# Optimization experiments

Measured on AMD Instinct MI355X. Metric: run time of the kernel, lower is better.

The kernel has to match this reference:

```python
import jax, jax.numpy as jnp
import numpy as np

EPS = 1e-7
BLOCK_SIZE = 128
LN_EPS = 1e-6

def _project(x):
    norm = jnp.maximum(jnp.linalg.norm(x, axis=-1, keepdims=True), EPS)
    max_norm = 1.0 - EPS
    return jnp.where(norm >= 1.0, x / norm * max_norm, x)

def _mobius_add(x, y, c):
    x2 = jnp.sum(x * x, -1, keepdims=True)
    y2 = jnp.sum(y * y, -1, keepdims=True)
    xy = jnp.sum(x * y, -1, keepdims=True)
    num = (1 + 2 * c * xy + c * y2) * x + (1 - c * x2) * y
    den = 1 + 2 * c * xy + c * c * x2 * y2
    return _project(num / jnp.maximum(den, EPS))

def _logmap0(y, c):
    sqrt_c = jnp.maximum(jnp.sqrt(c), EPS)
    y_norm = jnp.linalg.norm(y, axis=-1, keepdims=True)
    safe = jnp.maximum(y_norm, EPS)
    mag = jnp.arctanh(jnp.minimum(y_norm, 1.0 - EPS)) / sqrt_c
    return jnp.where(y_norm < EPS, jnp.zeros_like(y), mag * (y / safe))

def _expmap0(v, c):
    sqrt_c = jnp.maximum(jnp.sqrt(c), EPS)
    v_norm = jnp.linalg.norm(v, axis=-1, keepdims=True)
    safe = jnp.maximum(v_norm, EPS)
    mag = jnp.tanh(sqrt_c * safe) / sqrt_c
    return _project(jnp.where(v_norm < EPS, jnp.zeros_like(v), mag * (v / safe)))

def _dist(x, y, c):
    sqrt_c = jnp.maximum(jnp.sqrt(c), EPS)
    add_norm = jnp.linalg.norm(_mobius_add(-x, y, c), axis=-1)
    sc = jnp.squeeze(sqrt_c, -1)
    arg = jnp.minimum(sc * add_norm, 1.0 - EPS)
    return 2.0 * jnp.arctanh(arg) / sc

def _layernorm(t, scale, bias):
    mu = jnp.mean(t, -1, keepdims=True)
    var = jnp.mean((t - mu) ** 2, -1, keepdims=True)
    return (t - mu) * jax.lax.rsqrt(var + LN_EPS) * scale + bias

def _rope(x, fc):
    # x: [Be, H, bs, hd]; fc: [bs, hd//2] complex
    x_r, x_i = jnp.split(x, 2, -1)
    xc = jax.lax.complex(x_r, x_i)
    rot = xc * fc.reshape(1, 1, fc.shape[0], fc.shape[1])
    return jnp.concatenate([rot.real, rot.imag], -1)

def setup_inputs() -> dict:
    key = jax.random.key(0)
    ks = jax.random.split(key, 8)
    B, N, D, H = 1, 1024, 1024, 16
    w = lambda k, s: jax.random.normal(k, s, jnp.float32) * 0.02
    x = jax.random.normal(ks[0], (B, N, D), jnp.float32) * 0.02  # points inside the ball
    c_global = jax.random.uniform(ks[1], (B, 1), jnp.float32, minval=0.1, maxval=1.0)
    return dict(
        x=x, c_global=c_global,
        qkv_w=w(ks[2], (D, 3 * D)), qkv_b=jnp.zeros((3 * D,), jnp.float32),
        out_w=w(ks[3], (D, D)), out_b=jnp.zeros((D,), jnp.float32),
        ffn_w1=w(ks[4], (D, 4 * D)), ffn_b1=jnp.zeros((4 * D,), jnp.float32),
        ffn_w2=w(ks[5], (4 * D, D)), ffn_b2=jnp.zeros((D,), jnp.float32),
        ln1_scale=jnp.ones((D,), jnp.float32), ln1_bias=jnp.zeros((D,), jnp.float32),
        ln2_scale=jnp.ones((D,), jnp.float32), ln2_bias=jnp.zeros((D,), jnp.float32),
        c_logits=jnp.zeros((H,), jnp.float32),
        geo_scale=jnp.ones((1, H, 1, 1), jnp.float32),
        start_pos=0,
    )

def reference(x, c_global, qkv_w, qkv_b, out_w, out_b, ffn_w1, ffn_b1, ffn_w2, ffn_b2,
              ln1_scale, ln1_bias, ln2_scale, ln2_bias, c_logits, geo_scale, start_pos):
    B, N, D = x.shape
    H = c_logits.shape[0]
    hd = D // H
    bs = BLOCK_SIZE
    nb = N // bs
    Be = B * nb
    xb = x.reshape(Be, bs, D)
    c_b = jnp.repeat(c_global, nb, axis=0).reshape(Be, 1, 1)
    x_res1 = xb
    # tangent-space norm 1 + attention input
    x_norm = _expmap0(_layernorm(_logmap0(xb, c_b), ln1_scale, ln1_bias), c_b)
    x_tan = _logmap0(x_norm, c_b)
    qkv = (x_tan @ qkv_w + qkv_b).reshape(Be, bs, 3, H, hd).transpose(2, 0, 3, 1, 4)
    q, k, v = qkv[0], qkv[1], qkv[2]  # [Be, H, bs, hd]
    # block-local RoPE (module recomputes freqs_cis for h_dim/block_size internally)
    freqs = 1.0 / (10000.0 ** (jnp.arange(0, hd, 2, dtype=jnp.float32) / hd))
    fc = jnp.exp(1j * jnp.outer(jnp.arange(bs), freqs))
    q = _rope(q, fc)
    k = _rope(k, fc)
    c_head = jax.nn.softplus(c_logits).reshape(1, H, 1, 1)
    q_hyp = _expmap0(q, c_head)
    k_hyp = _expmap0(k, c_head)
    d = _dist(q_hyp[:, :, :, None, :], k_hyp[:, :, None, :, :], c_head[:, :, None, :, :])  # [Be,H,bs,bs]
    attn = jax.nn.softmax(-geo_scale * d, axis=-1)
    ao = jnp.einsum('bhqk,bhkd->bhqd', attn, v).transpose(0, 2, 1, 3).reshape(Be, bs, D)
    ao = ao @ out_w + out_b
    x_att = _mobius_add(x_res1, _expmap0(ao, c_b), c_b)
    # tangent-space norm 2 + hyperbolic FFN
    x_norm2 = _expmap0(_layernorm(_logmap0(x_att, c_b), ln2_scale, ln2_bias), c_b)
    t = _logmap0(x_norm2, c_b)
    t = jax.nn.gelu(t @ ffn_w1 + ffn_b1) @ ffn_w2 + ffn_b2
    x_ffn = _expmap0(t, c_b)
    out = _mobius_add(x_att, x_ffn, c_b)
    return out.reshape(B, N, D)
```

## Files before the change

kernel.cpp:

```cpp
#include <hip/hip_runtime.h>

typedef unsigned int uint;
typedef unsigned short ushort;
typedef __attribute__((ext_vector_type(8))) short bf16x8;
typedef __attribute__((ext_vector_type(4))) float f32x4;

#define EPSF 1e-7f
#define ONE_M_EPS 0.99999988079071044921875f
#define ATANH_1ME 8.4056213f
#define Y2_CLIP 0.99999982f

__device__ __forceinline__ ushort f2bf(float f){
  union{float f;uint u;}x; x.f=f; uint u=x.u;
  return (ushort)((u + 0x7fffu + ((u>>16)&1u)) >> 16);
}
__device__ __forceinline__ float bf2f(ushort u){
  union{uint u;float f;}x; x.u = ((uint)u)<<16; return x.f;
}
__device__ __forceinline__ float atanh_c(float a){
  a = fminf(a, ONE_M_EPS);
  return 0.5f*__logf((1.f+a)/(1.f-a));
}
__device__ __forceinline__ float gelu_t(float v){
  return 0.5f*v*(1.f + tanhf(0.7978845608f*(v + 0.044715f*v*v*v)));
}

__device__ __forceinline__ float expmap_factor(float n2, float sc, float& r2){
  float n = sqrtf(n2);
  if (n < EPSF) { r2 = 0.f; return 0.f; }
  float mag = tanhf(sc*n)/sc;
  float f = mag/n;
  if (mag >= 1.f) { f *= ONE_M_EPS/mag; r2 = Y2_CLIP; }
  else r2 = mag*mag;
  return f;
}
__device__ __forceinline__ float roundtrip_factor(float tn2, float sc){
  float tn = sqrtf(tn2);
  if (tn < EPSF) return 0.f;
  float mag = tanhf(sc*tn)/sc;
  if (mag >= 1.f) {
    return ATANH_1ME / (sc * tn);
  } else {
    if (mag < EPSF) return 0.f;
    return (mag/tn) * (atanh_c(mag) / (sc * mag));
  }
}

__device__ __constant__ float FREQS[32] = {
  1.0f, 0.7498942093324559f, 0.5623413251903491f, 0.4216965034285822f,
  0.31622776601683794f, 0.23713737056616552f, 0.1778279410038923f, 0.13335214321633242f,
  0.1f, 0.07498942093324558f, 0.05623413251903491f, 0.04216965034285822f,
  0.03162277660168379f, 0.023713737056616554f, 0.01778279410038923f, 0.013335214321633242f,
  0.01f, 0.007498942093324559f, 0.005623413251903491f, 0.004216965034285822f,
  0.0031622776601683794f, 0.0023713737056616554f, 0.0017782794100389228f, 0.0013335214321633241f,
  0.001f, 0.0007498942093324558f, 0.0005623413251903491f, 0.0004216965034285822f,
  0.00031622776601683794f, 0.00023713737056616553f, 0.00017782794100389227f, 0.00013335214321633243f
};

__device__ __forceinline__ void rope64(float* v, int row){
  #pragma unroll
  for (int i=0;i<32;i++){
    float sn, cn; __sincosf((float)row * FREQS[i], &sn, &cn);
    float a = v[i], b = v[i+32];
    v[i] = a*cn - b*sn;
    v[i+32] = a*sn + b*cn;
  }
}

__device__ __forceinline__ float blkSum(float v, float* tmp){
  #pragma unroll
  for (int o=32;o>0;o>>=1) v += __shfl_xor(v, o, 64);
  int w = threadIdx.x >> 6;
  if ((threadIdx.x & 63) == 0) tmp[w] = v;
  __syncthreads();
  v = tmp[0]+tmp[1]+tmp[2]+tmp[3];
  __syncthreads();
  return v;
}
__device__ __forceinline__ float2 blkSum2(float a, float b, float* tmp){
  #pragma unroll
  for (int o=32;o>0;o>>=1){ a += __shfl_xor(a, o, 64); b += __shfl_xor(b, o, 64); }
  int w = threadIdx.x >> 6;
  if ((threadIdx.x & 63) == 0){ tmp[w] = a; tmp[4+w] = b; }
  __syncthreads();
  float2 r; r.x = tmp[0]+tmp[1]+tmp[2]+tmp[3]; r.y = tmp[4]+tmp[5]+tmp[6]+tmp[7];
  __syncthreads();
  return r;
}

__global__ __launch_bounds__(256) void k_pre(const float* __restrict__ qkv_w,
    const float* __restrict__ out_w, const float* __restrict__ ffn_w1,
    const float* __restrict__ ffn_w2, const float* __restrict__ x,
    const float* __restrict__ cg, const float* __restrict__ lns, const float* __restrict__ lnb,
    ushort* __restrict__ wq, ushort* __restrict__ wo,
    ushort* __restrict__ w1, ushort* __restrict__ w2, ushort* __restrict__ xtan){
  __shared__ float s[32][33];
  int b = blockIdx.x;
  if (b < 12288){
    const float* W; ushort* WT; int K, N;
    if (b < 3072){ W=qkv_w; WT=wq; K=1024; N=3072; }
    else if (b < 4096){ b-=3072; W=out_w; WT=wo; K=1024; N=1024; }
    else if (b < 8192){ b-=4096; W=ffn_w1; WT=w1; K=1024; N=4096; }
    else { b-=8192; W=ffn_w2; WT=w2; K=4096; N=1024; }
    int nbn = N >> 5;
    int n0 = (b % nbn)*32, k0 = (b / nbn)*32;
    int tx = threadIdx.x & 31, ty = threadIdx.x >> 5;
    #pragma unroll
    for (int i=0;i<4;i++)
      s[ty+8*i][tx] = W[(size_t)(k0+ty+8*i)*N + n0+tx];
    __syncthreads();
    #pragma unroll
    for (int i=0;i<4;i++)
      WT[(size_t)(n0+ty+8*i)*K + k0+tx] = f2bf(s[tx][ty+8*i]);
  } else {
    float* tmp = &s[0][0];
    int r = b - 12288, t = threadIdx.x;
    float c = cg[0];
    float sc = fmaxf(sqrtf(c), EPSF);
    float4 xv = ((const float4*)(x + (size_t)r*1024))[t];
    float n2 = blkSum(xv.x*xv.x + xv.y*xv.y + xv.z*xv.z + xv.w*xv.w, tmp);
    float n = sqrtf(n2);
    float f1 = (n < EPSF) ? 0.f : (atanh_c(n) / sc / n);
    float ux = xv.x*f1, uy = xv.y*f1, uz = xv.z*f1, uw = xv.w*f1;
    float2 s12 = blkSum2(ux+uy+uz+uw, ux*ux+uy*uy+uz*uz+uw*uw, tmp);
    float mu = s12.x*(1.f/1024.f);
    float var = s12.y*(1.f/1024.f) - mu*mu;
    float inv = rsqrtf(var + 1e-6f);
    float4 sv = ((const float4*)lns)[t];
    float4 bv = ((const float4*)lnb)[t];
    float ta = (ux-mu)*inv*sv.x + bv.x;
    float tb = (uy-mu)*inv*sv.y + bv.y;
    float tc = (uz-mu)*inv*sv.z + bv.z;
    float td = (uw-mu)*inv*sv.w + bv.w;
    float tn2 = blkSum(ta*ta+tb*tb+tc*tc+td*td, tmp);
    float f = roundtrip_factor(tn2, sc);
    ushort4 o; o.x=f2bf(ta*f); o.y=f2bf(tb*f); o.z=f2bf(tc*f); o.w=f2bf(td*f);
    ((ushort4*)(xtan + (size_t)r*1024))[t] = o;
  }
}

template<int EPI>
__global__ __launch_bounds__(256) void k_gemm(const ushort* __restrict__ A,
    const ushort* __restrict__ Bt, const float* __restrict__ bias,
    void* __restrict__ C, int M, int N, int Kstride, int Kchunk){
  constexpr int MF = 2, NF = 4;
  __shared__ ushort As[2][128*64];
  __shared__ ushort Bs[2][64*64];
  const int tid = threadIdx.x;
  const int lane = tid & 63;
  const int wid = tid >> 6;
  const int ro = wid * 32, co = 0;
  const int l15 = lane & 15, hi = lane >> 4;
  const int nwg = gridDim.x * gridDim.y;
  const int lin = blockIdx.y * gridDim.x + blockIdx.x;
  const int qq = nwg >> 3, rr = nwg & 7;
  const int xcd = lin & 7, ii = lin >> 3;
  const int swz = (xcd < rr) ? (xcd*(qq+1) + ii) : (rr*(qq+1) + (xcd-rr)*qq + ii);
  const int m0 = (swz % gridDim.y) * 128;
  const int n0 = (swz / gridDim.y) * 64;
  const int z = blockIdx.z;
  const int kbase = z * Kchunk;
  const int swr = (l15 & 7) << 3;

  f32x4 acc[MF][NF];
  #pragma unroll
  for (int i=0;i<MF;i++)
    #pragma unroll
    for (int j=0;j<NF;j++) acc[i][j] = (f32x4){0.f,0.f,0.f,0.f};

  auto stage = [&](int buf, int koff){
    #pragma unroll
    for (int r2=0;r2<4;r2++){
      int idx = r2*256 + tid;
      int row = idx >> 3, cc = idx & 7;
      int off = koff + ((cc ^ (row & 7)) << 3);
      const ushort* ga = A + (size_t)(m0+row)*Kstride + off;
      int lo = (r2*256 + (tid & 192)) * 8;
      __builtin_amdgcn_global_load_lds((const __attribute__((address_space(1))) uint*)ga,
          (__attribute__((address_space(3))) uint*)&As[buf][lo], 16, 0, 0);
    }
    #pragma unroll
    for (int r2=0;r2<2;r2++){
      int idx = r2*256 + tid;
      int row = idx >> 3, cc = idx & 7;
      int off = koff + ((cc ^ (row & 7)) << 3);
      const ushort* gb = Bt + (size_t)(n0+row)*Kstride + off;
      int lo = (r2*256 + (tid & 192)) * 8;
      __builtin_amdgcn_global_load_lds((const __attribute__((address_space(1))) uint*)gb,
          (__attribute__((address_space(3))) uint*)&Bs[buf][lo], 16, 0, 0);
    }
  };
  auto compute = [&](int buf){
    #pragma unroll
    for (int ks=0;ks<2;ks++){
      bf16x8 af[MF], bfv[NF];
      int cb = (ks*32 + hi*8) ^ swr;
      #pragma unroll
      for (int m2=0;m2<MF;m2++) af[m2]  = *(const bf16x8*)&As[buf][(ro+m2*16+l15)*64 + cb];
      #pragma unroll
      for (int n2=0;n2<NF;n2++) bfv[n2] = *(const bf16x8*)&Bs[buf][(co+n2*16+l15)*64 + cb];
      #pragma unroll
      for (int m2=0;m2<MF;m2++)
        #pragma unroll
        for (int n2=0;n2<NF;n2++)
          acc[m2][n2] = __builtin_amdgcn_mfma_f32_16x16x32_bf16(af[m2], bfv[n2], acc[m2][n2], 0, 0, 0);
    }
  };

  const int nt = Kchunk >> 6;
  stage(0, kbase);
  __syncthreads();
  int cur = 0;
  for (int t = 1; t < nt; ++t){
    stage(cur ^ 1, kbase + t*64);
    compute(cur);
    __syncthreads();
    cur ^= 1;
  }
  compute(cur);

  #pragma unroll
  for (int m=0;m<MF;m++){
    #pragma unroll
    for (int n=0;n<NF;n++){
      int gc = n0 + co + n*16 + l15;
      float bb = (EPI == 3) ? (z == 0 ? bias[gc] : 0.f) : bias[gc];
      #pragma unroll
      for (int i=0;i<4;i++){
        int gr = m0 + ro + m*16 + hi*4 + i;
        float v = acc[m][n][i] + bb;
        if (EPI == 2) v = gelu_t(v);
        if (EPI == 2) ((ushort*)C)[(size_t)gr*N + gc] = f2bf(v);
        else ((float*)C)[(size_t)z*M*N + (size_t)gr*N + gc] = v;
      }
    }
  }
}

__global__ __launch_bounds__(256) void k_attn5(const float* __restrict__ qkv,
    const float* __restrict__ c_logits, const float* __restrict__ geo,
    ushort* __restrict__ ao){
  constexpr size_t PSTRIDE = (size_t)1024*3072;
  __shared__ ushort Kh[128*64], Kl[128*64];
  __shared__ ushort Vth[64*128];
  __shared__ ushort Qh[64*64], Ql[64*64];
  __shared__ float k2s[128], q2s[64];
  const int h = blockIdx.x, be = blockIdx.y, qs = blockIdx.z;
  const int tid = threadIdx.x;
  const float cl = c_logits[h];
  const float ch = (cl > 20.f) ? cl : log1pf(__expf(cl));
  const float sc = fmaxf(sqrtf(ch), EPSF);
  const float gs = geo[h];

  if (tid < 128){
    int kv = tid;
    const float4* pa = (const float4*)(qkv + (size_t)(be*128+kv)*3072 + 1024 + h*64);
    const float4* pb = (const float4*)(qkv + PSTRIDE + (size_t)(be*128+kv)*3072 + 1024 + h*64);
    float v[64];
    #pragma unroll
    for (int c=0;c<16;c++){
      float4 ta = pa[c], tb = pb[c];
      v[4*c]=ta.x+tb.x; v[4*c+1]=ta.y+tb.y; v[4*c+2]=ta.z+tb.z; v[4*c+3]=ta.w+tb.w;
    }
    rope64(v, kv);
    float n2 = 0.f;
    #pragma unroll
    for (int e=0;e<64;e++) n2 += v[e]*v[e];
    float r2; float f = expmap_factor(n2, sc, r2);
    k2s[kv] = r2;
    #pragma unroll
    for (int cch=0; cch<8; cch++){
      uint hw[4], lw[4];
      #pragma unroll
      for (int w2=0; w2<4; w2++){
        float a0 = v[cch*8 + w2*2] * f, a1 = v[cch*8 + w2*2 + 1] * f;
        ushort h0 = f2bf(a0); ushort l0 = f2bf(a0 - bf2f(h0));
        ushort h1 = f2bf(a1); ushort l1 = f2bf(a1 - bf2f(h1));
        hw[w2] = (uint)h0 | ((uint)h1<<16);
        lw[w2] = (uint)l0 | ((uint)l1<<16);
      }
      uint4 uh; uh.x=hw[0]; uh.y=hw[1]; uh.z=hw[2]; uh.w=hw[3];
      uint4 ul; ul.x=lw[0]; ul.y=lw[1]; ul.z=lw[2]; ul.w=lw[3];
      int idx = kv*64 + ((cch ^ (kv&7))<<3);
      *(uint4*)&Kh[idx] = uh;
      *(uint4*)&Kl[idx] = ul;
    }
  } else if (tid < 192){
    #pragma unroll
    for (int rr2=0; rr2<2; rr2++){
      int kv = (tid - 128) + rr2*64;
      const float4* pa = (const float4*)(qkv + (size_t)(be*128+kv)*3072 + 2048 + h*64);
      const float4* pb = (const float4*)(qkv + PSTRIDE + (size_t)(be*128+kv)*3072 + 2048 + h*64);
      float v[64];
      #pragma unroll
      for (int c=0;c<16;c++){
        float4 ta = pa[c], tb = pb[c];
        v[4*c]=ta.x+tb.x; v[4*c+1]=ta.y+tb.y; v[4*c+2]=ta.z+tb.z; v[4*c+3]=ta.w+tb.w;
      }
      #pragma unroll
      for (int d=0; d<64; d++){
        int idx = d*128 + (((kv>>3) ^ (d&7))<<3) + (kv&7);
        Vth[idx] = f2bf(v[d]);
      }
    }
  } else {
    int ql = tid - 192;
    int qrow = qs*64 + ql;
    const float4* pa = (const float4*)(qkv + (size_t)(be*128+qrow)*3072 + h*64);
    const float4* pb = (const float4*)(qkv + PSTRIDE + (size_t)(be*128+qrow)*3072 + h*64);
    float v[64];
    #pragma unroll
    for (int c=0;c<16;c++){
      float4 ta = pa[c], tb = pb[c];
      v[4*c]=ta.x+tb.x; v[4*c+1]=ta.y+tb.y; v[4*c+2]=ta.z+tb.z; v[4*c+3]=ta.w+tb.w;
    }
    rope64(v, qrow);
    float n2 = 0.f;
    #pragma unroll
    for (int e=0;e<64;e++) n2 += v[e]*v[e];
    float r2; float f = expmap_factor(n2, sc, r2);
    q2s[ql] = r2;
    #pragma unroll
    for (int cch=0; cch<8; cch++){
      uint hw[4], lw[4];
      #pragma unroll
      for (int w2=0; w2<4; w2++){
        float a0 = v[cch*8 + w2*2] * f, a1 = v[cch*8 + w2*2 + 1] * f;
        ushort h0 = f2bf(a0); ushort l0 = f2bf(a0 - bf2f(h0));
        ushort h1 = f2bf(a1); ushort l1 = f2bf(a1 - bf2f(h1));
        hw[w2] = (uint)h0 | ((uint)h1<<16);
        lw[w2] = (uint)l0 | ((uint)l1<<16);
      }
      uint4 uh; uh.x=hw[0]; uh.y=hw[1]; uh.z=hw[2]; uh.w=hw[3];
      uint4 ul; ul.x=lw[0]; ul.y=lw[1]; ul.z=lw[2]; ul.w=lw[3];
      int idx = ql*64 + ((cch ^ (ql&7))<<3);
      *(uint4*)&Qh[idx] = uh;
      *(uint4*)&Ql[idx] = ul;
    }
  }
  __syncthreads();

  const int lane = tid & 63, w = tid >> 6;
  const int l15 = lane & 15, hi4 = lane >> 4;
  f32x4 acc[8];
  #pragma unroll
  for (int nf=0;nf<8;nf++) acc[nf] = (f32x4){0.f,0.f,0.f,0.f};
  #pragma unroll
  for (int ks=0; ks<2; ks++){
    int qrowL = w*16 + l15;
    int qidx = qrowL*64 + (((ks*4 + hi4) ^ (qrowL&7))<<3);
    bf16x8 qh = *(const bf16x8*)&Qh[qidx];
    bf16x8 ql2 = *(const bf16x8*)&Ql[qidx];
    #pragma unroll
    for (int nf=0; nf<8; nf++){
      int krow = nf*16 + l15;
      int kidx = krow*64 + (((ks*4 + hi4) ^ (krow&7))<<3);
      bf16x8 kh = *(const bf16x8*)&Kh[kidx];
      bf16x8 kl2 = *(const bf16x8*)&Kl[kidx];
      acc[nf] = __builtin_amdgcn_mfma_f32_16x16x32_bf16(qh, kh, acc[nf], 0, 0, 0);
      acc[nf] = __builtin_amdgcn_mfma_f32_16x16x32_bf16(qh, kl2, acc[nf], 0, 0, 0);
      acc[nf] = __builtin_amdgcn_mfma_f32_16x16x32_bf16(ql2, kh, acc[nf], 0, 0, 0);
    }
  }
  __syncthreads();

  float q2v[4], Bfv[4];
  #pragma unroll
  for (int i=0;i<4;i++){ q2v[i] = q2s[w*16 + hi4*4 + i]; Bfv[i] = 1.f - ch*q2v[i]; }
  const float e2 = 2.f*ch;
  #pragma unroll
  for (int nf=0; nf<8; nf++){
    float k2 = k2s[nf*16 + l15];
    #pragma unroll
    for (int i=0;i<4;i++){
      float xy = acc[nf][i];
      float Af = 1.f + ch*k2 - e2*xy;
      float den = fmaxf(Af - ch*k2*Bfv[i], EPSF);
      float num2 = fmaxf(Af*(Af*q2v[i] - 2.f*Bfv[i]*xy) + Bfv[i]*Bfv[i]*k2, 0.f);
      float rn = sqrtf(num2)/den;
      rn = (rn >= 1.f) ? ONE_M_EPS : rn;
      float arg = fminf(sc*rn, ONE_M_EPS);
      float dd = __logf((1.f+arg)/(1.f-arg)) / sc;
      acc[nf][i] = -gs*dd;
    }
  }
  #pragma unroll
  for (int i=0;i<4;i++){
    float m = acc[0][i];
    #pragma unroll
    for (int nf=1;nf<8;nf++) m = fmaxf(m, acc[nf][i]);
    #pragma unroll
    for (int o=1;o<16;o<<=1) m = fmaxf(m, __shfl_xor(m, o));
    float l = 0.f;
    #pragma unroll
    for (int nf=0;nf<8;nf++){ float pp = __expf(acc[nf][i]-m); acc[nf][i] = pp; l += pp; }
    #pragma unroll
    for (int o=1;o<16;o<<=1) l += __shfl_xor(l, o);
    float inv = 1.f/l;
    #pragma unroll
    for (int nf=0;nf<8;nf++){
      float p = acc[nf][i]*inv;
      ushort ph = f2bf(p);
      ushort pl = f2bf(p - bf2f(ph));
      int row = w*16 + hi4*4 + i, col = nf*16 + l15;
      int idx = row*128 + (((col>>3) ^ (row&7))<<3) + (col&7);
      Kh[idx] = ph; Kl[idx] = pl;
    }
  }
  __syncthreads();

  f32x4 acc2[4];
  #pragma unroll
  for (int nf=0;nf<4;nf++) acc2[nf] = (f32x4){0.f,0.f,0.f,0.f};
  #pragma unroll
  for (int ks=0; ks<4; ks++){
    int prow = w*16 + l15;
    int pidx = prow*128 + (((ks*4 + hi4) ^ (prow&7))<<3);
    bf16x8 ph = *(const bf16x8*)&Kh[pidx];
    bf16x8 pl = *(const bf16x8*)&Kl[pidx];
    #pragma unroll
    for (int nf=0; nf<4; nf++){
      int vrow = nf*16 + l15;
      int vidx = vrow*128 + (((ks*4 + hi4) ^ (vrow&7))<<3);
      bf16x8 vh = *(const bf16x8*)&Vth[vidx];
      acc2[nf] = __builtin_amdgcn_mfma_f32_16x16x32_bf16(ph, vh, acc2[nf], 0, 0, 0);
      acc2[nf] = __builtin_amdgcn_mfma_f32_16x16x32_bf16(pl, vh, acc2[nf], 0, 0, 0);
    }
  }
  #pragma unroll
  for (int nf=0; nf<4; nf++)
    #pragma unroll
    for (int i=0;i<4;i++){
      int row = qs*64 + w*16 + hi4*4 + i;
      int col = nf*16 + l15;
      ao[(size_t)(be*128 + row)*1024 + h*64 + col] = f2bf(acc2[nf][i]);
    }
}

__global__ __launch_bounds__(256) void k_postattn(const float* __restrict__ x,
    const float* __restrict__ proj, const float* __restrict__ cg,
    const float* __restrict__ lns, const float* __restrict__ lnb,
    float* __restrict__ xatt, ushort* __restrict__ tout){
  __shared__ float tmp[8];
  int r = blockIdx.x, t = threadIdx.x;
  float c = cg[0], sc = fmaxf(sqrtf(c), EPSF);
  float4 pa = ((const float4*)(proj + (size_t)r*1024))[t];
  float4 pb = ((const float4*)(proj + 1024*1024 + (size_t)r*1024))[t];
  float4 pc = ((const float4*)(proj + 2*1024*1024 + (size_t)r*1024))[t];
  float4 pd = ((const float4*)(proj + 3*1024*1024 + (size_t)r*1024))[t];
  float4 pv; pv.x=(pa.x+pb.x)+(pc.x+pd.x); pv.y=(pa.y+pb.y)+(pc.y+pd.y);
  pv.z=(pa.z+pb.z)+(pc.z+pd.z); pv.w=(pa.w+pb.w)+(pc.w+pd.w);
  float4 xv = ((const float4*)(x + (size_t)r*1024))[t];
  float pn2 = blkSum(pv.x*pv.x+pv.y*pv.y+pv.z*pv.z+pv.w*pv.w, tmp);
  float y2; float fy = expmap_factor(pn2, sc, y2);
  float ya = pv.x*fy, yb = pv.y*fy, yc = pv.z*fy, yd = pv.w*fy;
  float2 s = blkSum2(xv.x*xv.x+xv.y*xv.y+xv.z*xv.z+xv.w*xv.w,
                     xv.x*ya+xv.y*yb+xv.z*yc+xv.w*yd, tmp);
  float x2 = s.x, xy = s.y;
  float Af = 1.f + 2.f*c*xy + c*y2;
  float Bf = 1.f - c*x2;
  float den = fmaxf(1.f + 2.f*c*xy + c*c*x2*y2, EPSF);
  float num2 = fmaxf(Af*Af*x2 + 2.f*Af*Bf*xy + Bf*Bf*y2, 0.f);
  float rn = sqrtf(num2)/den;
  float fp = (rn >= 1.f) ? (ONE_M_EPS/fmaxf(rn,EPSF)) : 1.f;
  float xan = (rn >= 1.f) ? ONE_M_EPS : rn;
  float g = fp/den;
  float xa = (Af*xv.x + Bf*ya)*g;
  float xb = (Af*xv.y + Bf*yb)*g;
  float xc = (Af*xv.z + Bf*yc)*g;
  float xd = (Af*xv.w + Bf*yd)*g;
  float4 xo; xo.x=xa; xo.y=xb; xo.z=xc; xo.w=xd;
  ((float4*)(xatt + (size_t)r*1024))[t] = xo;
  float at = (rn >= 1.f) ? ATANH_1ME : atanh_c(xan);
  float fl = (xan < EPSF) ? 0.f : at / sc / fmaxf(xan, EPSF);
  float ux = xa*fl, uy = xb*fl, uz = xc*fl, uw = xd*fl;
  float2 s12 = blkSum2(ux+uy+uz+uw, ux*ux+uy*uy+uz*uz+uw*uw, tmp);
  float mu = s12.x*(1.f/1024.f);
  float var = s12.y*(1.f/1024.f) - mu*mu;
  float inv = rsqrtf(var + 1e-6f);
  float4 sv = ((const float4*)lns)[t];
  float4 bv = ((const float4*)lnb)[t];
  float ta = (ux-mu)*inv*sv.x + bv.x;
  float tb = (uy-mu)*inv*sv.y + bv.y;
  float tc = (uz-mu)*inv*sv.z + bv.z;
  float td = (uw-mu)*inv*sv.w + bv.w;
  float tn2 = blkSum(ta*ta+tb*tb+tc*tc+td*td, tmp);
  float f = roundtrip_factor(tn2, sc);
  ushort4 o; o.x=f2bf(ta*f); o.y=f2bf(tb*f); o.z=f2bf(tc*f); o.w=f2bf(td*f);
  ((ushort4*)(tout + (size_t)r*1024))[t] = o;
}

__global__ __launch_bounds__(256) void k_final(const float* __restrict__ xatt,
    const float* __restrict__ tf, const float* __restrict__ cg, float* __restrict__ out){
  __shared__ float tmp[8];
  int r = blockIdx.x, t = threadIdx.x;
  float c = cg[0], sc = fmaxf(sqrtf(c), EPSF);
  float4 fa = ((const float4*)(tf + (size_t)r*1024))[t];
  float4 fb = ((const float4*)(tf + 1024*1024 + (size_t)r*1024))[t];
  float4 fc = ((const float4*)(tf + 2*1024*1024 + (size_t)r*1024))[t];
  float4 fd = ((const float4*)(tf + 3*1024*1024 + (size_t)r*1024))[t];
  float4 fv; fv.x=(fa.x+fb.x)+(fc.x+fd.x); fv.y=(fa.y+fb.y)+(fc.y+fd.y);
  fv.z=(fa.z+fb.z)+(fc.z+fd.z); fv.w=(fa.w+fb.w)+(fc.w+fd.w);
  float4 xv = ((const float4*)(xatt + (size_t)r*1024))[t];
  float fn2 = blkSum(fv.x*fv.x+fv.y*fv.y+fv.z*fv.z+fv.w*fv.w, tmp);
  float y2; float fy = expmap_factor(fn2, sc, y2);
  float ya = fv.x*fy, yb = fv.y*fy, yc = fv.z*fy, yd = fv.w*fy;
  float2 s = blkSum2(xv.x*xv.x+xv.y*xv.y+xv.z*xv.z+xv.w*xv.w,
                     xv.x*ya+xv.y*yb+xv.z*yc+xv.w*yd, tmp);
  float x2 = s.x, xy = s.y;
  float Af = 1.f + 2.f*c*xy + c*y2;
  float Bf = 1.f - c*x2;
  float den = fmaxf(1.f + 2.f*c*xy + c*c*x2*y2, EPSF);
  float num2 = fmaxf(Af*Af*x2 + 2.f*Af*Bf*xy + Bf*Bf*y2, 0.f);
  float rn = sqrtf(num2)/den;
  float fp = (rn >= 1.f) ? (ONE_M_EPS/fmaxf(rn,EPSF)) : 1.f;
  float g = fp/den;
  float4 o;
  o.x = (Af*xv.x + Bf*ya)*g;
  o.y = (Af*xv.y + Bf*yb)*g;
  o.z = (Af*xv.z + Bf*yc)*g;
  o.w = (Af*xv.w + Bf*yd)*g;
  ((float4*)(out + (size_t)r*1024))[t] = o;
}

extern "C" void kernel_launch(void* const* d_in, const int* in_sizes, int n_in,
                              void* d_out, int out_size, void* d_ws, size_t ws_size,
                              hipStream_t stream){
  (void)in_sizes; (void)n_in; (void)out_size; (void)ws_size;
  const float* x     = (const float*)d_in[0];
  const float* cg    = (const float*)d_in[1];
  const float* qkv_w = (const float*)d_in[2];
  const float* qkv_b = (const float*)d_in[3];
  const float* out_w = (const float*)d_in[4];
  const float* out_b = (const float*)d_in[5];
  const float* ffn_w1= (const float*)d_in[6];
  const float* ffn_b1= (const float*)d_in[7];
  const float* ffn_w2= (const float*)d_in[8];
  const float* ffn_b2= (const float*)d_in[9];
  const float* ln1s  = (const float*)d_in[10];
  const float* ln1b  = (const float*)d_in[11];
  const float* ln2s  = (const float*)d_in[12];
  const float* ln2b  = (const float*)d_in[13];
  const float* clog  = (const float*)d_in[14];
  const float* geo   = (const float*)d_in[15];

  char* p = (char*)d_ws;
  auto take = [&](size_t n){ char* r = p; p += (n + 255) & ~(size_t)255; return r; };
  ushort* wt_qkv  = (ushort*)take((size_t)3072*1024*2);
  ushort* wt_out  = (ushort*)take((size_t)1024*1024*2);
  ushort* wt_ffn1 = (ushort*)take((size_t)4096*1024*2);
  ushort* wt_ffn2 = (ushort*)take((size_t)1024*4096*2);
  float*  bufA    = (float*)take((size_t)2*1024*3072*4);
  ushort* bufB    = (ushort*)take((size_t)1024*1024*2);
  float*  bufC    = (float*)take((size_t)4*1024*1024*4);
  float*  xatt    = (float*)take((size_t)1024*1024*4);
  ushort* tbuf    = (ushort*)take((size_t)1024*1024*2);

  k_pre<<<13312, 256, 0, stream>>>(qkv_w, out_w, ffn_w1, ffn_w2, x, cg, ln1s, ln1b,
                                   wt_qkv, wt_out, wt_ffn1, wt_ffn2, bufB);
  k_gemm<3><<<dim3(48,8,2), 256, 0, stream>>>(bufB, wt_qkv, qkv_b, (void*)bufA, 1024, 3072, 1024, 512);
  k_attn5<<<dim3(16,8,2), 256, 0, stream>>>(bufA, clog, geo, bufB);
  k_gemm<3><<<dim3(16,8,4), 256, 0, stream>>>(bufB, wt_out, out_b, (void*)bufC, 1024, 1024, 1024, 256);
  k_postattn<<<1024, 256, 0, stream>>>(x, bufC, cg, ln2s, ln2b, xatt, tbuf);
  k_gemm<2><<<dim3(64,8,1), 256, 0, stream>>>(tbuf, wt_ffn1, ffn_b1, (void*)bufA, 1024, 4096, 1024, 1024);
  k_gemm<3><<<dim3(16,8,4), 256, 0, stream>>>((const ushort*)bufA, wt_ffn2, ffn_b2, (void*)bufC, 1024, 1024, 4096, 1024);
  k_final<<<1024, 256, 0, stream>>>(xatt, bufC, cg, (float*)d_out);
}
```

Before: 116.6 us.

## Fuse RoPE, expmap and hi/lo split into QKV GEMM epilogue

The QKV GEMM drops its split-K of 2 and gains an epilogue that adds bias, applies RoPE, computes per-row norms with the expmap scale, and writes Q/K as bf16 hi/lo pairs plus V as bf16 in per-head layouts. The attention kernel then loads these tiles straight into LDS with global_load_lds instead of reading and summing two fp32 partial buffers and redoing the preprocessing. This removes the fp32 QKV round trip and the duplicated per-block Q/K work. In exchange the GEMM epilogue gets heavier, its stores are scattered 2-byte writes, and the GEMM loses the parallelism of split-K.

```diff
diff --git a/kernel.cpp b/kernel.cpp
--- a/kernel.cpp
+++ b/kernel.cpp
@@ -56,16 +56,6 @@
   0.001f, 0.0007498942093324558f, 0.0005623413251903491f, 0.0004216965034285822f,
   0.00031622776601683794f, 0.00023713737056616553f, 0.00017782794100389227f, 0.00013335214321633243f
 };
-
-__device__ __forceinline__ void rope64(float* v, int row){
-  #pragma unroll
-  for (int i=0;i<32;i++){
-    float sn, cn; __sincosf((float)row * FREQS[i], &sn, &cn);
-    float a = v[i], b = v[i+32];
-    v[i] = a*cn - b*sn;
-    v[i+32] = a*sn + b*cn;
-  }
-}
 
 __device__ __forceinline__ float blkSum(float v, float* tmp){
   #pragma unroll
@@ -142,14 +132,18 @@
 template<int EPI>
 __global__ __launch_bounds__(256) void k_gemm(const ushort* __restrict__ A,
     const ushort* __restrict__ Bt, const float* __restrict__ bias,
-    void* __restrict__ C, int M, int N, int Kstride, int Kchunk){
+    void* __restrict__ C, int M, int N, int Kstride, int Kchunk,
+    ushort* __restrict__ qhg, ushort* __restrict__ qlg,
+    ushort* __restrict__ khg, ushort* __restrict__ klg,
+    ushort* __restrict__ vhg, float* __restrict__ q2g, float* __restrict__ k2g,
+    const float* __restrict__ clog){
   constexpr int MF = 2, NF = 4;
   __shared__ ushort As[2][128*64];
   __shared__ ushort Bs[2][64*64];
   const int tid = threadIdx.x;
   const int lane = tid & 63;
   const int wid = tid >> 6;
-  const int ro = wid * 32, co = 0;
+  const int ro = wid * 32;
   const int l15 = lane & 15, hi = lane >> 4;
   const int nwg = gridDim.x * gridDim.y;
   const int lin = blockIdx.y * gridDim.x + blockIdx.x;
@@ -198,7 +192,7 @@
       #pragma unroll
       for (int m2=0;m2<MF;m2++) af[m2]  = *(const bf16x8*)&As[buf][(ro+m2*16+l15)*64 + cb];
       #pragma unroll
-      for (int n2=0;n2<NF;n2++) bfv[n2] = *(const bf16x8*)&Bs[buf][(co+n2*16+l15)*64 + cb];
+      for (int n2=0;n2<NF;n2++) bfv[n2] = *(const bf16x8*)&Bs[buf][(n2*16+l15)*64 + cb];
       #pragma unroll
       for (int m2=0;m2<MF;m2++)
         #pragma unroll
@@ -219,28 +213,103 @@
   }
   compute(cur);
 
+  if (EPI == 4){
+    float v[MF][NF][4];
+    #pragma unroll
+    for (int m2=0;m2<MF;m2++)
+      #pragma unroll
+      for (int n2=0;n2<NF;n2++){
+        float bb = bias[n0 + n2*16 + l15];
+        #pragma unroll
+        for (int i=0;i<4;i++) v[m2][n2][i] = acc[m2][n2][i] + bb;
+      }
+    const int type = n0 >> 10;
+    const int h = (n0 & 1023) >> 6;
+    if (type < 2){
+      #pragma unroll
+      for (int m2=0;m2<MF;m2++)
+        #pragma unroll
+        for (int i=0;i<4;i++){
+          int gr = m0 + ro + m2*16 + hi*4 + i;
+          float r = (float)(gr & 127);
+          #pragma unroll
+          for (int pp=0;pp<2;pp++){
+            int d = pp*16 + l15;
+            float sn, cn; __sincosf(r * FREQS[d], &sn, &cn);
+            float a = v[m2][pp][i], b = v[m2][pp+2][i];
+            v[m2][pp][i]   = a*cn - b*sn;
+            v[m2][pp+2][i] = a*sn + b*cn;
+          }
+        }
+      const float cl = clog[h];
+      const float chh = (cl > 20.f) ? cl : log1pf(__expf(cl));
+      const float sch = fmaxf(sqrtf(chh), EPSF);
+      ushort* hdst = (type==0) ? qhg : khg;
+      ushort* ldst = (type==0) ? qlg : klg;
+      float*  sdst = (type==0) ? q2g : k2g;
+      #pragma unroll
+      for (int m2=0;m2<MF;m2++)
+        #pragma unroll
+        for (int i=0;i<4;i++){
+          float n2s = 0.f;
+          #pragma unroll
+          for (int n2=0;n2<NF;n2++) n2s += v[m2][n2][i]*v[m2][n2][i];
+          #pragma unroll
+          for (int o=1;o<16;o<<=1) n2s += __shfl_xor(n2s, o);
+          float r2; float f = expmap_factor(n2s, sch, r2);
+          int gr = m0 + ro + m2*16 + hi*4 + i;
+          int be = gr >> 7, r = gr & 127;
+          size_t rowbase = ((size_t)(be*16 + h)*128 + r)*64;
+          #pragma unroll
+          for (int n2=0;n2<NF;n2++){
+            float val = v[m2][n2][i]*f;
+            ushort hb = f2bf(val);
+            ushort lb = f2bf(val - bf2f(hb));
+            hdst[rowbase + n2*16 + l15] = hb;
+            ldst[rowbase + n2*16 + l15] = lb;
+          }
+          if (l15 == 0) sdst[(size_t)(be*16+h)*128 + r] = r2;
+        }
+    } else {
+      #pragma unroll
+      for (int m2=0;m2<MF;m2++)
+        #pragma unroll
+        for (int i=0;i<4;i++){
+          int gr = m0 + ro + m2*16 + hi*4 + i;
+          int be = gr >> 7, r = gr & 127;
+          size_t rowbase = ((size_t)(be*16 + h)*128 + r)*64;
+          #pragma unroll
+          for (int n2=0;n2<NF;n2++)
+            vhg[rowbase + n2*16 + l15] = f2bf(v[m2][n2][i]);
+        }
+    }
+    return;
+  }
+
   #pragma unroll
   for (int m=0;m<MF;m++){
     #pragma unroll
     for (int n=0;n<NF;n++){
-      int gc = n0 + co + n*16 + l15;
+      int gc = n0 + n*16 + l15;
       float bb = (EPI == 3) ? (z == 0 ? bias[gc] : 0.f) : bias[gc];
       #pragma unroll
       for (int i=0;i<4;i++){
         int gr = m0 + ro + m*16 + hi*4 + i;
-        float v = acc[m][n][i] + bb;
-        if (EPI == 2) v = gelu_t(v);
-        if (EPI == 2) ((ushort*)C)[(size_t)gr*N + gc] = f2bf(v);
-        else ((float*)C)[(size_t)z*M*N + (size_t)gr*N + gc] = v;
+        float v2 = acc[m][n][i] + bb;
+        if (EPI == 2) v2 = gelu_t(v2);
+        if (EPI == 2) ((ushort*)C)[(size_t)gr*N + gc] = f2bf(v2);
+        else ((float*)C)[(size_t)z*M*N + (size_t)gr*N + gc] = v2;
       }
     }
   }
 }
 
-__global__ __launch_bounds__(256) void k_attn5(const float* __restrict__ qkv,
+__global__ __launch_bounds__(256) void k_attn6(const ushort* __restrict__ qhg,
+    const ushort* __restrict__ qlg, const ushort* __restrict__ khg,
+    const ushort* __restrict__ klg, const ushort* __restrict__ vhg,
+    const float* __restrict__ q2g, const float* __restrict__ k2g,
     const float* __restrict__ c_logits, const float* __restrict__ geo,
     ushort* __restrict__ ao){
-  constexpr size_t PSTRIDE = (size_t)1024*3072;
   __shared__ ushort Kh[128*64], Kl[128*64];
   __shared__ ushort Vth[64*128];
   __shared__ ushort Qh[64*64], Ql[64*64];
@@ -251,92 +320,45 @@
   const float ch = (cl > 20.f) ? cl : log1pf(__expf(cl));
   const float sc = fmaxf(sqrtf(ch), EPSF);
   const float gs = geo[h];
-
+  const size_t tbase = (size_t)(be*16 + h)*8192;
+
+  #pragma unroll
+  for (int r2=0;r2<4;r2++){
+    int idx = r2*256 + tid;
+    int row = idx >> 3, cc = idx & 7;
+    int off = row*64 + ((cc ^ (row & 7)) << 3);
+    int lo = (r2*256 + (tid & 192)) * 8;
+    __builtin_amdgcn_global_load_lds((const __attribute__((address_space(1))) uint*)(khg + tbase + off),
+        (__attribute__((address_space(3))) uint*)&Kh[lo], 16, 0, 0);
+    __builtin_amdgcn_global_load_lds((const __attribute__((address_space(1))) uint*)(klg + tbase + off),
+        (__attribute__((address_space(3))) uint*)&Kl[lo], 16, 0, 0);
+  }
+  #pragma unroll
+  for (int r2=0;r2<2;r2++){
+    int idx = r2*256 + tid;
+    int row = idx >> 3, cc = idx & 7;
+    int off = (qs*64 + row)*64 + ((cc ^ (row & 7)) << 3);
+    int lo = (r2*256 + (tid & 192)) * 8;
+    __builtin_amdgcn_global_load_lds((const __attribute__((address_space(1))) uint*)(qhg + tbase + off),
+        (__attribute__((address_space(3))) uint*)&Qh[lo], 16, 0, 0);
+    __builtin_amdgcn_global_load_lds((const __attribute__((address_space(1))) uint*)(qlg + tbase + off),
+        (__attribute__((address_space(3))) uint*)&Ql[lo], 16, 0, 0);
+  }
   if (tid < 128){
     int kv = tid;
-    const float4* pa = (const float4*)(qkv + (size_t)(be*128+kv)*3072 + 1024 + h*64);
-    const float4* pb = (const float4*)(qkv + PSTRIDE + (size_t)(be*128+kv)*3072 + 1024 + h*64);
-    float v[64];
-    #pragma unroll
-    for (int c=0;c<16;c++){
-      float4 ta = pa[c], tb = pb[c];
-      v[4*c]=ta.x+tb.x; v[4*c+1]=ta.y+tb.y; v[4*c+2]=ta.z+tb.z; v[4*c+3]=ta.w+tb.w;
-    }
-    rope64(v, kv);
-    float n2 = 0.f;
-    #pragma unroll
-    for (int e=0;e<64;e++) n2 += v[e]*v[e];
-    float r2; float f = expmap_factor(n2, sc, r2);
-    k2s[kv] = r2;
-    #pragma unroll
-    for (int cch=0; cch<8; cch++){
-      uint hw[4], lw[4];
-      #pragma unroll
-      for (int w2=0; w2<4; w2++){
-        float a0 = v[cch*8 + w2*2] * f, a1 = v[cch*8 + w2*2 + 1] * f;
-        ushort h0 = f2bf(a0); ushort l0 = f2bf(a0 - bf2f(h0));
-        ushort h1 = f2bf(a1); ushort l1 = f2bf(a1 - bf2f(h1));
-        hw[w2] = (uint)h0 | ((uint)h1<<16);
-        lw[w2] = (uint)l0 | ((uint)l1<<16);
-      }
-      uint4 uh; uh.x=hw[0]; uh.y=hw[1]; uh.z=hw[2]; uh.w=hw[3];
-      uint4 ul; ul.x=lw[0]; ul.y=lw[1]; ul.z=lw[2]; ul.w=lw[3];
-      int idx = kv*64 + ((cch ^ (kv&7))<<3);
-      *(uint4*)&Kh[idx] = uh;
-      *(uint4*)&Kl[idx] = ul;
-    }
+    const uint4* src = (const uint4*)(vhg + tbase + kv*64);
+    ushort v[64];
+    #pragma unroll
+    for (int c2=0;c2<8;c2++) *(uint4*)&v[c2*8] = src[c2];
+    #pragma unroll
+    for (int d=0; d<64; d++){
+      int idx = d*128 + (((kv>>3) ^ (d&7))<<3) + (kv&7);
+      Vth[idx] = v[d];
+    }
+    k2s[kv] = k2g[(size_t)(be*16+h)*128 + kv];
   } else if (tid < 192){
-    #pragma unroll
-    for (int rr2=0; rr2<2; rr2++){
-      int kv = (tid - 128) + rr2*64;
-      const float4* pa = (const float4*)(qkv + (size_t)(be*128+kv)*3072 + 2048 + h*64);
-      const float4* pb = (const float4*)(qkv + PSTRIDE + (size_t)(be*128+kv)*3072 + 2048 + h*64);
-      float v[64];
-      #pragma unroll
-      for (int c=0;c<16;c++){
-        float4 ta = pa[c], tb = pb[c];
-        v[4*c]=ta.x+tb.x; v[4*c+1]=ta.y+tb.y; v[4*c+2]=ta.z+tb.z; v[4*c+3]=ta.w+tb.w;
-      }
-      #pragma unroll
-      for (int d=0; d<64; d++){
-        int idx = d*128 + (((kv>>3) ^ (d&7))<<3) + (kv&7);
-        Vth[idx] = f2bf(v[d]);
-      }
-    }
-  } else {
-    int ql = tid - 192;
-    int qrow = qs*64 + ql;
-    const float4* pa = (const float4*)(qkv + (size_t)(be*128+qrow)*3072 + h*64);
-    const float4* pb = (const float4*)(qkv + PSTRIDE + (size_t)(be*128+qrow)*3072 + h*64);
-    float v[64];
-    #pragma unroll
-    for (int c=0;c<16;c++){
-      float4 ta = pa[c], tb = pb[c];
-      v[4*c]=ta.x+tb.x; v[4*c+1]=ta.y+tb.y; v[4*c+2]=ta.z+tb.z; v[4*c+3]=ta.w+tb.w;
-    }
-    rope64(v, qrow);
-    float n2 = 0.f;
-    #pragma unroll
-    for (int e=0;e<64;e++) n2 += v[e]*v[e];
-    float r2; float f = expmap_factor(n2, sc, r2);
-    q2s[ql] = r2;
-    #pragma unroll
-    for (int cch=0; cch<8; cch++){
-      uint hw[4], lw[4];
-      #pragma unroll
-      for (int w2=0; w2<4; w2++){
-        float a0 = v[cch*8 + w2*2] * f, a1 = v[cch*8 + w2*2 + 1] * f;
-        ushort h0 = f2bf(a0); ushort l0 = f2bf(a0 - bf2f(h0));
-        ushort h1 = f2bf(a1); ushort l1 = f2bf(a1 - bf2f(h1));
-        hw[w2] = (uint)h0 | ((uint)h1<<16);
-        lw[w2] = (uint)l0 | ((uint)l1<<16);
-      }
-      uint4 uh; uh.x=hw[0]; uh.y=hw[1]; uh.z=hw[2]; uh.w=hw[3];
-      uint4 ul; ul.x=lw[0]; ul.y=lw[1]; ul.z=lw[2]; ul.w=lw[3];
-      int idx = ql*64 + ((cch ^ (ql&7))<<3);
-      *(uint4*)&Qh[idx] = uh;
-      *(uint4*)&Ql[idx] = ul;
-    }
+    int i2 = tid - 128;
+    q2s[i2] = q2g[(size_t)(be*16+h)*128 + qs*64 + i2];
   }
   __syncthreads();
 
@@ -550,19 +572,30 @@
   ushort* wt_out  = (ushort*)take((size_t)1024*1024*2);
   ushort* wt_ffn1 = (ushort*)take((size_t)4096*1024*2);
   ushort* wt_ffn2 = (ushort*)take((size_t)1024*4096*2);
-  float*  bufA    = (float*)take((size_t)2*1024*3072*4);
+  float*  bufA    = (float*)take((size_t)1024*4096*4);
   ushort* bufB    = (ushort*)take((size_t)1024*1024*2);
   float*  bufC    = (float*)take((size_t)4*1024*1024*4);
   float*  xatt    = (float*)take((size_t)1024*1024*4);
   ushort* tbuf    = (ushort*)take((size_t)1024*1024*2);
+  ushort* qhg     = (ushort*)take((size_t)1024*1024*2);
+  ushort* qlg     = (ushort*)take((size_t)1024*1024*2);
+  ushort* khg     = (ushort*)take((size_t)1024*1024*2);
+  ushort* klg     = (ushort*)take((size_t)1024*1024*2);
+  ushort* vhg     = (ushort*)take((size_t)1024*1024*2);
+  float*  q2g     = (float*)take((size_t)16384*4);
+  float*  k2g     = (float*)take((size_t)16384*4);
 
   k_pre<<<13312, 256, 0, stream>>>(qkv_w, out_w, ffn_w1, ffn_w2, x, cg, ln1s, ln1b,
                                    wt_qkv, wt_out, wt_ffn1, wt_ffn2, bufB);
-  k_gemm<3><<<dim3(48,8,2), 256, 0, stream>>>(bufB, wt_qkv, qkv_b, (void*)bufA, 1024, 3072, 1024, 512);
-  k_attn5<<<dim3(16,8,2), 256, 0, stream>>>(bufA, clog, geo, bufB);
-  k_gemm<3><<<dim3(16,8,4), 256, 0, stream>>>(bufB, wt_out, out_b, (void*)bufC, 1024, 1024, 1024, 256);
+  k_gemm<4><<<dim3(48,8,1), 256, 0, stream>>>(bufB, wt_qkv, qkv_b, nullptr, 1024, 3072, 1024, 1024,
+                                              qhg, qlg, khg, klg, vhg, q2g, k2g, clog);
+  k_attn6<<<dim3(16,8,2), 256, 0, stream>>>(qhg, qlg, khg, klg, vhg, q2g, k2g, clog, geo, bufB);
+  k_gemm<3><<<dim3(16,8,4), 256, 0, stream>>>(bufB, wt_out, out_b, (void*)bufC, 1024, 1024, 1024, 256,
+                                              nullptr,nullptr,nullptr,nullptr,nullptr,nullptr,nullptr,nullptr);
   k_postattn<<<1024, 256, 0, stream>>>(x, bufC, cg, ln2s, ln2b, xatt, tbuf);
-  k_gemm<2><<<dim3(64,8,1), 256, 0, stream>>>(tbuf, wt_ffn1, ffn_b1, (void*)bufA, 1024, 4096, 1024, 1024);
-  k_gemm<3><<<dim3(16,8,4), 256, 0, stream>>>((const ushort*)bufA, wt_ffn2, ffn_b2, (void*)bufC, 1024, 1024, 4096, 1024);
+  k_gemm<2><<<dim3(64,8,1), 256, 0, stream>>>(tbuf, wt_ffn1, ffn_b1, (void*)bufA, 1024, 4096, 1024, 1024,
+                                              nullptr,nullptr,nullptr,nullptr,nullptr,nullptr,nullptr,nullptr);
+  k_gemm<3><<<dim3(16,8,4), 256, 0, stream>>>((const ushort*)bufA, wt_ffn2, ffn_b2, (void*)bufC, 1024, 1024, 4096, 1024,
+                                              nullptr,nullptr,nullptr,nullptr,nullptr,nullptr,nullptr,nullptr);
   k_final<<<1024, 256, 0, stream>>>(xatt, bufC, cg, (float*)d_out);
 }
```

New measurement: 121.4 us. 1.04x slower.
